# Optimization experiments

Measured on AMD Instinct MI355X. Metric: run time of the kernel, lower is better.

## Reference

```python
import jax, jax.numpy as jnp
import numpy as np

V, H, B, S, L = 32000, 512, 256, 128, 5
KAIMING_STD = float(np.sqrt(2.0 / H))  # kaiming_normal_ on (B,H): fan_in=H, gain=sqrt(2)
UNIF = float(1.0 / np.sqrt(H))         # torch LSTMCell/Linear default init scale


def setup_inputs() -> dict:
    key = jax.random.key(0)
    ks = jax.random.split(key, 12)
    x = jax.random.randint(ks[0], (B, S), 0, V)
    h0 = jax.random.normal(ks[1], (L, B, H), jnp.float32) * KAIMING_STD
    c0 = jax.random.normal(ks[2], (L, B, H), jnp.float32) * KAIMING_STD
    emb = jax.random.normal(ks[3], (V, H), jnp.float32)
    emb = emb.at[0].set(0.0)  # padding_idx=0
    W_ih = jax.random.uniform(ks[4], (L, 4 * H, H), jnp.float32, -UNIF, UNIF)
    W_hh = jax.random.uniform(ks[5], (L, 4 * H, H), jnp.float32, -UNIF, UNIF)
    b_ih = jax.random.uniform(ks[6], (L, 4 * H), jnp.float32, -UNIF, UNIF)
    b_hh = jax.random.uniform(ks[7], (L, 4 * H), jnp.float32, -UNIF, UNIF)
    W_out = jax.random.uniform(ks[8], (V, H), jnp.float32, -UNIF, UNIF)
    b_out = jax.random.uniform(ks[9], (V,), jnp.float32, -UNIF, UNIF)
    return {"x": x, "h0": h0, "c0": c0, "emb": emb, "W_ih": W_ih, "W_hh": W_hh,
            "b_ih": b_ih, "b_hh": b_hh, "W_out": W_out, "b_out": b_out}


def reference(x, h0, c0, emb, W_ih, W_hh, b_ih, b_hh, W_out, b_out):
    e = emb[x]                      # (B, S, H)
    seq = e.reshape(S, B, H)        # faithful replica of torch .view(S, B, -1) memory reinterpretation

    def step(carry, xt):
        h, c = carry                # each (L, B, H)
        inp = xt
        hs, cs = [], []
        for l in range(L):
            gates = inp @ W_ih[l].T + b_ih[l] + h[l] @ W_hh[l].T + b_hh[l]  # (B, 4H)
            i, f, g, o = jnp.split(gates, 4, axis=-1)
            i = jax.nn.sigmoid(i)
            f = jax.nn.sigmoid(f)
            g = jnp.tanh(g)
            o = jax.nn.sigmoid(o)
            cn = f * c[l] + i * g
            hn = o * jnp.tanh(cn)
            hs.append(hn)
            cs.append(cn)
            inp = hn
        return (jnp.stack(hs), jnp.stack(cs)), None

    (h, c), _ = jax.lax.scan(step, (h0, c0), seq)
    return h[L - 1] @ W_out.T + b_out  # (B, V)
```

## Files before the change

kernel.cpp:

```cpp
#include <hip/hip_runtime.h>
#include <hip/hip_bf16.h>

#define VOCAB 32000
#define HID 512
#define BATCH 256
#define SEQ 128
#define NL 5
#define BH (BATCH*HID)
#define G4H (4*HID)
#define NBLK 160

typedef __attribute__((ext_vector_type(8))) short short8;
typedef __attribute__((ext_vector_type(4))) float float4v;
typedef __attribute__((ext_vector_type(4))) unsigned int uint4v;

__device__ __forceinline__ float sigmoid_f(float x) {
    return 1.f / (1.f + __expf(-x));
}
__device__ __forceinline__ float tanh_f(float x) {
    float ax = fabsf(x);
    float e = __expf(2.f * ax);
    float t = 1.f - 2.f / (e + 1.f);
    return copysignf(t, x);
}
__device__ __forceinline__ short bf16bits(float f) {
    union { __hip_bfloat16 b; short s; } u;
    u.b = __float2bfloat16(f);
    return u.s;
}
__device__ __forceinline__ short8 load8f(const float* p) {
    float4v lo = *(const float4v*)p;
    float4v hi = *(const float4v*)(p + 4);
    short8 r;
    r[0] = bf16bits(lo[0]); r[1] = bf16bits(lo[1]);
    r[2] = bf16bits(lo[2]); r[3] = bf16bits(lo[3]);
    r[4] = bf16bits(hi[0]); r[5] = bf16bits(hi[1]);
    r[6] = bf16bits(hi[2]); r[7] = bf16bits(hi[3]);
    return r;
}
__device__ __forceinline__ short8 load8b(const __hip_bfloat16* p) {
    return *(const short8*)p;
}

#if __has_builtin(__builtin_amdgcn_make_buffer_rsrc) && \
    __has_builtin(__builtin_amdgcn_raw_buffer_load_b128) && \
    __has_builtin(__builtin_amdgcn_raw_buffer_store_b128)
#define USE_BUFFER_OPS 1
typedef __amdgpu_buffer_rsrc_t srd_t;
__device__ __forceinline__ srd_t make_srd(const void* p) {
    return __builtin_amdgcn_make_buffer_rsrc(const_cast<void*>(p), (short)0,
                                             0xFFFFFFFFu, 0x00020000);
}
__device__ __forceinline__ short8 bload16(srd_t srd, int voff, int soff) {
    union { uint4v u; short8 s; } c;
    c.u = __builtin_amdgcn_raw_buffer_load_b128(srd, voff, soff, 17);
    return c.s;
}
__device__ __forceinline__ void bstore16(short8 v, srd_t srd, int voff) {
    union { uint4v u; short8 s; } c; c.s = v;
    __builtin_amdgcn_raw_buffer_store_b128(c.u, srd, voff, 0, 17);
}
#else
#define USE_BUFFER_OPS 0
typedef const char* srd_t;
__device__ __forceinline__ srd_t make_srd(const void* p) {
    return (const char*)p;
}
__device__ __forceinline__ short8 bload16(srd_t srd, int voff, int soff) {
    const char* base = srd + voff + soff;
    union { unsigned long long q[2]; short8 s; } u;
    u.q[0] = __hip_atomic_load((const unsigned long long*)base,
                               __ATOMIC_RELAXED, __HIP_MEMORY_SCOPE_AGENT);
    u.q[1] = __hip_atomic_load((const unsigned long long*)(base + 8),
                               __ATOMIC_RELAXED, __HIP_MEMORY_SCOPE_AGENT);
    return u.s;
}
__device__ __forceinline__ void bstore16(short8 v, srd_t srd, int voff) {
    char* base = const_cast<char*>(srd) + voff;
    union { unsigned long long q[2]; short8 s; } u; u.s = v;
    __hip_atomic_store((unsigned long long*)base, u.q[0],
                       __ATOMIC_RELAXED, __HIP_MEMORY_SCOPE_AGENT);
    __hip_atomic_store((unsigned long long*)(base + 8), u.q[1],
                       __ATOMIC_RELAXED, __HIP_MEMORY_SCOPE_AGENT);
}
#endif

__device__ __forceinline__ size_t hidx(int p, int l, int j, int m, int c) {
    return ((((size_t)p * NL + l) * 32 + j) * 256 + m) * 16 + c;
}

__global__ void init_state_k(const float* __restrict__ h0,
                             __hip_bfloat16* __restrict__ hbuf,
                             int* __restrict__ done) {
    int i = blockIdx.x * 256 + threadIdx.x;
    int l = i / BH, r = i % BH;
    int m = r >> 9, col = r & 511;
    hbuf[hidx(1, l, col >> 4, m, col & 15)] = __float2bfloat16(h0[i]);
    if (blockIdx.x == 0 && threadIdx.x < NL) done[threadIdx.x * 64] = 0;
}

__global__ __launch_bounds__(1024) void lstm_persist_k(
    const int* __restrict__ x,
    const float* __restrict__ emb,
    const float* __restrict__ W_ih,
    const float* __restrict__ W_hh,
    const float* __restrict__ b_ih,
    const float* __restrict__ b_hh,
    const float* __restrict__ c0,
    __hip_bfloat16* __restrict__ hbuf,
    int* __restrict__ done)
{
    __shared__ short lw[65536];
    __shared__ short8 xch[16][32];

    const int tid = threadIdx.x;
    const int xcd = blockIdx.x & 7;
    const int ixc = blockIdx.x >> 3;
    const int slot = xcd * 20 + ixc;
    const int l = slot >> 5;
    const int j = slot & 31;
    const int jbase = j << 4;

    const int wave = tid >> 6, lane = tid & 63;
    const int quad = lane >> 4, l16 = lane & 15;
    const int m16 = wave << 4;

    const float* Wg[2] = { W_ih + (size_t)l * G4H * HID,
                           W_hh + (size_t)l * G4H * HID };

    for (int e = tid; e < 8192; e += 1024) {
        int row = e >> 6;
        int kc  = (e & 63) << 3;
        int gemm = row >> 6, r2 = row & 63, g = r2 >> 4, rl = r2 & 15;
        const float* src = Wg[gemm] + (size_t)(g * HID + jbase + rl) * HID + kc;
        short8 v = load8f(src);
        int kt = kc >> 5, q = (kc >> 3) & 3;
        int fragslot = ((gemm * 4 + g) * 16 + kt) * 64 + (q * 16 + rl);
        *(short8*)&lw[(size_t)fragslot * 8] = v;
    }

    const int jj = jbase + l16;
    float bias[4], c_r[4];
#pragma unroll
    for (int g = 0; g < 4; ++g)
        bias[g] = b_ih[l * G4H + g * HID + jj] + b_hh[l * G4H + g * HID + jj];
#pragma unroll
    for (int r = 0; r < 4; ++r)
        c_r[r] = c0[(size_t)l * BH + (size_t)(m16 + quad * 4 + r) * HID + jj];

    const short* lwb = lw + (size_t)lane * 8;
    const int shi = quad >> 1;
    const int abyte = (int)(((m16 + l16) * 16 + (quad & 1) * 8) * 2)
                    + shi * 8192;
    const srd_t hsrd = make_srd(hbuf);

    __syncthreads();

    for (int t = 0; t < SEQ; ++t) {
        if (tid == 0) {
            if (l > 0) {
                int need = 32 * (t + 1);
                while (__hip_atomic_load(&done[(l - 1) * 64], __ATOMIC_RELAXED,
                                         __HIP_MEMORY_SCOPE_AGENT) < need)
                    __builtin_amdgcn_s_sleep(1);
            }
            if (t > 0) {
                int need = 32 * t;
                while (__hip_atomic_load(&done[l * 64], __ATOMIC_RELAXED,
                                         __HIP_MEMORY_SCOPE_AGENT) < need)
                    __builtin_amdgcn_s_sleep(1);
            }
            if (l < NL - 1 && t >= 2) {
                int need = 32 * (t - 1);
                while (__hip_atomic_load(&done[(l + 1) * 64], __ATOMIC_RELAXED,
                                         __HIP_MEMORY_SCOPE_AGENT) < need)
                    __builtin_amdgcn_s_sleep(1);
            }
        }
        __syncthreads();

        const int p = t & 1, pm1 = p ^ 1;
        const int vpr = (int)(2 * hidx(pm1, l, 0, 0, 0)) + abyte;

        float4v acc[4];
#pragma unroll
        for (int g = 0; g < 4; ++g) acc[g] = (float4v){0.f, 0.f, 0.f, 0.f};

        if (l == 0) {
            int tok = x[t * BATCH + m16 + l16];
            const float* ar = emb + (size_t)tok * HID;
            short8 ah[4];
#pragma unroll
            for (int d = 0; d < 4; ++d)
                ah[d] = bload16(hsrd, vpr, d * 16384);
#pragma unroll
            for (int kt = 0; kt < 16; ++kt) {
                short8 a_in = load8f(ar + kt * 32 + quad * 8);
                short8 a_h = ah[kt & 3];
                if (kt + 4 < 16)
                    ah[kt & 3] = bload16(hsrd, vpr, (kt + 4) * 16384);
#pragma unroll
                for (int g = 0; g < 4; ++g) {
                    short8 b0 = *(const short8*)(lwb + (size_t)(g * 16 + kt) * 512);
                    short8 b1 = *(const short8*)(lwb + (size_t)((4 + g) * 16 + kt) * 512);
                    acc[g] = __builtin_amdgcn_mfma_f32_16x16x32_bf16(a_in, b0, acc[g], 0, 0, 0);
                    acc[g] = __builtin_amdgcn_mfma_f32_16x16x32_bf16(a_h,  b1, acc[g], 0, 0, 0);
                }
            }
        } else {
            const int vin = (int)(2 * hidx(p, l - 1, 0, 0, 0)) + abyte;
            short8 ai[4], ah[4];
#pragma unroll
            for (int d = 0; d < 4; ++d) {
                ai[d] = bload16(hsrd, vin, d * 16384);
                ah[d] = bload16(hsrd, vpr, d * 16384);
            }
#pragma unroll
            for (int kt = 0; kt < 16; ++kt) {
                short8 a_in = ai[kt & 3];
                short8 a_h  = ah[kt & 3];
                if (kt + 4 < 16) {
                    ai[kt & 3] = bload16(hsrd, vin, (kt + 4) * 16384);
                    ah[kt & 3] = bload16(hsrd, vpr, (kt + 4) * 16384);
                }
#pragma unroll
                for (int g = 0; g < 4; ++g) {
                    short8 b0 = *(const short8*)(lwb + (size_t)(g * 16 + kt) * 512);
                    short8 b1 = *(const short8*)(lwb + (size_t)((4 + g) * 16 + kt) * 512);
                    acc[g] = __builtin_amdgcn_mfma_f32_16x16x32_bf16(a_in, b0, acc[g], 0, 0, 0);
                    acc[g] = __builtin_amdgcn_mfma_f32_16x16x32_bf16(a_h,  b1, acc[g], 0, 0, 0);
                }
            }
        }

        short* xp = (short*)&xch[wave];
#pragma unroll
        for (int r = 0; r < 4; ++r) {
            float iv = sigmoid_f(acc[0][r] + bias[0]);
            float fv = sigmoid_f(acc[1][r] + bias[1]);
            float gv = tanh_f(acc[2][r] + bias[2]);
            float ov = sigmoid_f(acc[3][r] + bias[3]);
            c_r[r] = fv * c_r[r] + iv * gv;
            xp[(quad * 4 + r) * 16 + l16] = bf16bits(ov * tanh_f(c_r[r]));
        }
        __builtin_amdgcn_wave_barrier();
        if (lane < 32) {
            short8 v = *(const short8*)&xp[lane * 8];
            int vout = (int)(2 * hidx(p, l, j, m16, 0)) + lane * 16;
            bstore16(v, hsrd, vout);
        }

        __syncthreads();
        if (tid == 0)
            __hip_atomic_fetch_add(&done[l * 64], 1, __ATOMIC_RELEASE,
                                   __HIP_MEMORY_SCOPE_AGENT);
    }
}

__global__ __launch_bounds__(512) void out_gemm_k(
    const __hip_bfloat16* __restrict__ hbuf,
    const float* __restrict__ W_out,
    const float* __restrict__ b_out,
    float* __restrict__ out)
{
    const int nb = blockIdx.x;
    const int tid = threadIdx.x;
    const int wave = tid >> 6, lane = tid & 63;
    const int quad = lane >> 4, l16 = lane & 15;
    const int nt = wave & 3, mh = wave >> 2;

    const __hip_bfloat16* hfin = hbuf + hidx(1, NL - 1, 0, 0, 0);
    const int shi = quad >> 1;
    const size_t coff = (size_t)(quad & 1) * 8;

    const int ncol = nb * 64 + nt * 16 + l16;
    const float* brow = W_out + (size_t)ncol * HID;

    float4v acc[8];
#pragma unroll
    for (int mt = 0; mt < 8; ++mt) acc[mt] = (float4v){0.f, 0.f, 0.f, 0.f};

#pragma unroll 2
    for (int kt = 0; kt < 16; ++kt) {
        short8 b = load8f(brow + kt * 32 + quad * 8);
        const __hip_bfloat16* abase =
            hfin + (size_t)(2 * kt + shi) * 4096 + coff;
#pragma unroll
        for (int mt = 0; mt < 8; ++mt) {
            short8 a = load8b(abase + (size_t)(mh * 128 + mt * 16 + l16) * 16);
            acc[mt] = __builtin_amdgcn_mfma_f32_16x16x32_bf16(a, b, acc[mt], 0, 0, 0);
        }
    }

    float bo = b_out[ncol];
#pragma unroll
    for (int mt = 0; mt < 8; ++mt) {
#pragma unroll
        for (int r = 0; r < 4; ++r) {
            int m = mh * 128 + mt * 16 + quad * 4 + r;
            out[(size_t)m * VOCAB + ncol] = acc[mt][r] + bo;
        }
    }
}

extern "C" void kernel_launch(void* const* d_in, const int* in_sizes, int n_in,
                              void* d_out, int out_size, void* d_ws, size_t ws_size,
                              hipStream_t stream) {
    const int* x        = (const int*)d_in[0];
    const float* h0     = (const float*)d_in[1];
    const float* c0     = (const float*)d_in[2];
    const float* emb    = (const float*)d_in[3];
    const float* W_ih   = (const float*)d_in[4];
    const float* W_hh   = (const float*)d_in[5];
    const float* b_ih   = (const float*)d_in[6];
    const float* b_hh   = (const float*)d_in[7];
    const float* W_out  = (const float*)d_in[8];
    const float* b_out  = (const float*)d_in[9];
    float* out          = (float*)d_out;

    __hip_bfloat16* hbuf = (__hip_bfloat16*)d_ws;
    int* done = (int*)((char*)d_ws + (size_t)2 * NL * BH * sizeof(__hip_bfloat16));

    init_state_k<<<(NL * BH) / 256, 256, 0, stream>>>(h0, hbuf, done);

    lstm_persist_k<<<NBLK, 1024, 0, stream>>>(x, emb, W_ih, W_hh, b_ih, b_hh,
                                              c0, hbuf, done);

    out_gemm_k<<<VOCAB / 64, 512, 0, stream>>>(hbuf, W_out, b_out, out);
}
```

Before: 3.196 ms.

## Store per-timestep hidden states to drop downstream-layer backpressure wait

Measured after the change: 3.014 ms. 5.7% less time.

```diff
diff --git a/kernel.cpp b/kernel.cpp
--- a/kernel.cpp
+++ b/kernel.cpp
@@ -45,7 +45,6 @@
 #if __has_builtin(__builtin_amdgcn_make_buffer_rsrc) && \
     __has_builtin(__builtin_amdgcn_raw_buffer_load_b128) && \
     __has_builtin(__builtin_amdgcn_raw_buffer_store_b128)
-#define USE_BUFFER_OPS 1
 typedef __amdgpu_buffer_rsrc_t srd_t;
 __device__ __forceinline__ srd_t make_srd(const void* p) {
     return __builtin_amdgcn_make_buffer_rsrc(const_cast<void*>(p), (short)0,
@@ -61,7 +60,6 @@
     __builtin_amdgcn_raw_buffer_store_b128(c.u, srd, voff, 0, 17);
 }
 #else
-#define USE_BUFFER_OPS 0
 typedef const char* srd_t;
 __device__ __forceinline__ srd_t make_srd(const void* p) {
     return (const char*)p;
@@ -85,20 +83,31 @@
 }
 #endif
 
-__device__ __forceinline__ size_t hidx(int p, int l, int j, int m, int c) {
-    return ((((size_t)p * NL + l) * 32 + j) * 256 + m) * 16 + c;
+__host__ __device__ constexpr size_t hidx(int s, int l, int j, int m, int c) {
+    return ((((size_t)s * NL + l) * 32 + j) * 256 + m) * 16 + c;
+}
+
+template<int BIGWS>
+__device__ __forceinline__ short8 hload(const __hip_bfloat16* hbuf, srd_t srd,
+                                        size_t off, int d) {
+    if constexpr (BIGWS) {
+        return *(const short8*)((const char*)hbuf + off + (size_t)d * 16384);
+    } else {
+        return bload16(srd, (int)off, d * 16384);
+    }
 }
 
 __global__ void init_state_k(const float* __restrict__ h0,
                              __hip_bfloat16* __restrict__ hbuf,
-                             int* __restrict__ done) {
+                             int* __restrict__ done, int islot) {
     int i = blockIdx.x * 256 + threadIdx.x;
     int l = i / BH, r = i % BH;
     int m = r >> 9, col = r & 511;
-    hbuf[hidx(1, l, col >> 4, m, col & 15)] = __float2bfloat16(h0[i]);
+    hbuf[hidx(islot, l, col >> 4, m, col & 15)] = __float2bfloat16(h0[i]);
     if (blockIdx.x == 0 && threadIdx.x < NL) done[threadIdx.x * 64] = 0;
 }
 
+template<int BIGWS>
 __global__ __launch_bounds__(1024) void lstm_persist_k(
     const int* __restrict__ x,
     const float* __restrict__ emb,
@@ -150,8 +159,8 @@
 
     const short* lwb = lw + (size_t)lane * 8;
     const int shi = quad >> 1;
-    const int abyte = (int)(((m16 + l16) * 16 + (quad & 1) * 8) * 2)
-                    + shi * 8192;
+    const size_t abyte = (size_t)(((m16 + l16) * 16 + (quad & 1) * 8) * 2)
+                       + (size_t)shi * 8192;
     const srd_t hsrd = make_srd(hbuf);
 
     __syncthreads();
@@ -170,17 +179,23 @@
                                          __HIP_MEMORY_SCOPE_AGENT) < need)
                     __builtin_amdgcn_s_sleep(1);
             }
-            if (l < NL - 1 && t >= 2) {
-                int need = 32 * (t - 1);
-                while (__hip_atomic_load(&done[(l + 1) * 64], __ATOMIC_RELAXED,
-                                         __HIP_MEMORY_SCOPE_AGENT) < need)
-                    __builtin_amdgcn_s_sleep(1);
+            if constexpr (!BIGWS) {
+                if (l < NL - 1 && t >= 2) {
+                    int need = 32 * (t - 1);
+                    while (__hip_atomic_load(&done[(l + 1) * 64], __ATOMIC_RELAXED,
+                                             __HIP_MEMORY_SCOPE_AGENT) < need)
+                        __builtin_amdgcn_s_sleep(1);
+                }
             }
         }
         __syncthreads();
 
         const int p = t & 1, pm1 = p ^ 1;
-        const int vpr = (int)(2 * hidx(pm1, l, 0, 0, 0)) + abyte;
+        const int rslot_prev = BIGWS ? t : pm1;
+        const int rslot_in   = BIGWS ? (t + 1) : p;
+        const int wslot      = BIGWS ? (t + 1) : p;
+
+        const size_t vpr = 2 * hidx(rslot_prev, l, 0, 0, 0) + abyte;
 
         float4v acc[4];
 #pragma unroll
@@ -192,13 +207,13 @@
             short8 ah[4];
 #pragma unroll
             for (int d = 0; d < 4; ++d)
-                ah[d] = bload16(hsrd, vpr, d * 16384);
+                ah[d] = hload<BIGWS>(hbuf, hsrd, vpr, d);
 #pragma unroll
             for (int kt = 0; kt < 16; ++kt) {
                 short8 a_in = load8f(ar + kt * 32 + quad * 8);
                 short8 a_h = ah[kt & 3];
                 if (kt + 4 < 16)
-                    ah[kt & 3] = bload16(hsrd, vpr, (kt + 4) * 16384);
+                    ah[kt & 3] = hload<BIGWS>(hbuf, hsrd, vpr, kt + 4);
 #pragma unroll
                 for (int g = 0; g < 4; ++g) {
                     short8 b0 = *(const short8*)(lwb + (size_t)(g * 16 + kt) * 512);
@@ -208,20 +223,20 @@
                 }
             }
         } else {
-            const int vin = (int)(2 * hidx(p, l - 1, 0, 0, 0)) + abyte;
+            const size_t vin = 2 * hidx(rslot_in, l - 1, 0, 0, 0) + abyte;
             short8 ai[4], ah[4];
 #pragma unroll
             for (int d = 0; d < 4; ++d) {
-                ai[d] = bload16(hsrd, vin, d * 16384);
-                ah[d] = bload16(hsrd, vpr, d * 16384);
+                ai[d] = hload<BIGWS>(hbuf, hsrd, vin, d);
+                ah[d] = hload<BIGWS>(hbuf, hsrd, vpr, d);
             }
 #pragma unroll
             for (int kt = 0; kt < 16; ++kt) {
                 short8 a_in = ai[kt & 3];
                 short8 a_h  = ah[kt & 3];
                 if (kt + 4 < 16) {
-                    ai[kt & 3] = bload16(hsrd, vin, (kt + 4) * 16384);
-                    ah[kt & 3] = bload16(hsrd, vpr, (kt + 4) * 16384);
+                    ai[kt & 3] = hload<BIGWS>(hbuf, hsrd, vin, kt + 4);
+                    ah[kt & 3] = hload<BIGWS>(hbuf, hsrd, vpr, kt + 4);
                 }
 #pragma unroll
                 for (int g = 0; g < 4; ++g) {
@@ -246,7 +261,7 @@
         __builtin_amdgcn_wave_barrier();
         if (lane < 32) {
             short8 v = *(const short8*)&xp[lane * 8];
-            int vout = (int)(2 * hidx(p, l, j, m16, 0)) + lane * 16;
+            int vout = (int)(2 * hidx(wslot, l, j, m16, 0)) + lane * 16;
             bstore16(v, hsrd, vout);
         }
 
@@ -258,7 +273,7 @@
 }
 
 __global__ __launch_bounds__(512) void out_gemm_k(
-    const __hip_bfloat16* __restrict__ hbuf,
+    const __hip_bfloat16* __restrict__ hfin,
     const float* __restrict__ W_out,
     const float* __restrict__ b_out,
     float* __restrict__ out)
@@ -269,7 +284,6 @@
     const int quad = lane >> 4, l16 = lane & 15;
     const int nt = wave & 3, mh = wave >> 2;
 
-    const __hip_bfloat16* hfin = hbuf + hidx(1, NL - 1, 0, 0, 0);
     const int shi = quad >> 1;
     const size_t coff = (size_t)(quad & 1) * 8;
 
@@ -319,12 +333,23 @@
     float* out          = (float*)d_out;
 
     __hip_bfloat16* hbuf = (__hip_bfloat16*)d_ws;
-    int* done = (int*)((char*)d_ws + (size_t)2 * NL * BH * sizeof(__hip_bfloat16));
-
-    init_state_k<<<(NL * BH) / 256, 256, 0, stream>>>(h0, hbuf, done);
-
-    lstm_persist_k<<<NBLK, 1024, 0, stream>>>(x, emb, W_ih, W_hh, b_ih, b_hh,
-                                              c0, hbuf, done);
-
-    out_gemm_k<<<VOCAB / 64, 512, 0, stream>>>(hbuf, W_out, b_out, out);
-}
+
+    const size_t hbytes_big = (size_t)(SEQ + 1) * NL * BH * sizeof(__hip_bfloat16);
+    const bool big = ws_size >= hbytes_big + 4096;
+
+    if (big) {
+        int* done = (int*)((char*)d_ws + hbytes_big);
+        init_state_k<<<(NL * BH) / 256, 256, 0, stream>>>(h0, hbuf, done, 0);
+        lstm_persist_k<1><<<NBLK, 1024, 0, stream>>>(x, emb, W_ih, W_hh, b_ih,
+                                                     b_hh, c0, hbuf, done);
+        out_gemm_k<<<VOCAB / 64, 512, 0, stream>>>(
+            hbuf + hidx(SEQ, NL - 1, 0, 0, 0), W_out, b_out, out);
+    } else {
+        int* done = (int*)((char*)d_ws + (size_t)2 * NL * BH * sizeof(__hip_bfloat16));
+        init_state_k<<<(NL * BH) / 256, 256, 0, stream>>>(h0, hbuf, done, 1);
+        lstm_persist_k<0><<<NBLK, 1024, 0, stream>>>(x, emb, W_ih, W_hh, b_ih,
+                                                     b_hh, c0, hbuf, done);
+        out_gemm_k<<<VOCAB / 64, 512, 0, stream>>>(
+            hbuf + hidx(1, NL - 1, 0, 0, 0), W_out, b_out, out);
+    }
+}
```

## Assign LSTM layers to XCDs dynamically and keep recurrent state in XCD-local L2

Applied to the files above, without the earlier changes.

Measured after the change: 3.569 ms. 11.6% more time.

```diff
diff --git a/kernel.cpp b/kernel.cpp
--- a/kernel.cpp
+++ b/kernel.cpp
@@ -8,7 +8,15 @@
 #define NL 5
 #define BH (BATCH*HID)
 #define G4H (4*HID)
-#define NBLK 160
+#define NBLK_LAUNCH 256
+
+#define LAYB  (32*256*16*2)
+#define SLOTB (NL*LAYB)
+
+#define F_DONE(l)   ((l)*64)
+#define F_CLAIM(x)  (384 + (x)*8)
+#define F_CHECKIN   512
+#define F_SPILL     576
 
 typedef __attribute__((ext_vector_type(8))) short short8;
 typedef __attribute__((ext_vector_type(4))) float float4v;
@@ -45,7 +53,6 @@
 #if __has_builtin(__builtin_amdgcn_make_buffer_rsrc) && \
     __has_builtin(__builtin_amdgcn_raw_buffer_load_b128) && \
     __has_builtin(__builtin_amdgcn_raw_buffer_store_b128)
-#define USE_BUFFER_OPS 1
 typedef __amdgpu_buffer_rsrc_t srd_t;
 __device__ __forceinline__ srd_t make_srd(const void* p) {
     return __builtin_amdgcn_make_buffer_rsrc(const_cast<void*>(p), (short)0,
@@ -56,12 +63,16 @@
     c.u = __builtin_amdgcn_raw_buffer_load_b128(srd, voff, soff, 17);
     return c.s;
 }
+__device__ __forceinline__ short8 bload16_l2(srd_t srd, int voff, int soff) {
+    union { uint4v u; short8 s; } c;
+    c.u = __builtin_amdgcn_raw_buffer_load_b128(srd, voff, soff, 1);
+    return c.s;
+}
 __device__ __forceinline__ void bstore16(short8 v, srd_t srd, int voff) {
     union { uint4v u; short8 s; } c; c.s = v;
     __builtin_amdgcn_raw_buffer_store_b128(c.u, srd, voff, 0, 17);
 }
 #else
-#define USE_BUFFER_OPS 0
 typedef const char* srd_t;
 __device__ __forceinline__ srd_t make_srd(const void* p) {
     return (const char*)p;
@@ -75,6 +86,9 @@
                                __ATOMIC_RELAXED, __HIP_MEMORY_SCOPE_AGENT);
     return u.s;
 }
+__device__ __forceinline__ short8 bload16_l2(srd_t srd, int voff, int soff) {
+    return bload16(srd, voff, soff);
+}
 __device__ __forceinline__ void bstore16(short8 v, srd_t srd, int voff) {
     char* base = const_cast<char*>(srd) + voff;
     union { unsigned long long q[2]; short8 s; } u; u.s = v;
@@ -85,18 +99,181 @@
 }
 #endif
 
-__device__ __forceinline__ size_t hidx(int p, int l, int j, int m, int c) {
-    return ((((size_t)p * NL + l) * 32 + j) * 256 + m) * 16 + c;
+__host__ __device__ constexpr size_t hidx(int s, int l, int j, int m, int c) {
+    return ((((size_t)s * NL + l) * 32 + j) * 256 + m) * 16 + c;
 }
 
 __global__ void init_state_k(const float* __restrict__ h0,
                              __hip_bfloat16* __restrict__ hbuf,
-                             int* __restrict__ done) {
+                             __hip_bfloat16* __restrict__ hloc,
+                             int* __restrict__ flags) {
     int i = blockIdx.x * 256 + threadIdx.x;
     int l = i / BH, r = i % BH;
     int m = r >> 9, col = r & 511;
-    hbuf[hidx(1, l, col >> 4, m, col & 15)] = __float2bfloat16(h0[i]);
-    if (blockIdx.x == 0 && threadIdx.x < NL) done[threadIdx.x * 64] = 0;
+    size_t o = hidx(1, l, col >> 4, m, col & 15);
+    __hip_bfloat16 v = __float2bfloat16(h0[i]);
+    hbuf[o] = v;
+    hloc[o] = v;
+    if (blockIdx.x == 0) {
+        flags[threadIdx.x] = 0;
+        flags[threadIdx.x + 256] = 0;
+        flags[threadIdx.x + 512] = 0;
+    }
+}
+
+template<int FAST>
+__device__ __forceinline__ void lstm_run(
+    const int* __restrict__ x, const float* __restrict__ emb,
+    const float* __restrict__ W_ih, const float* __restrict__ W_hh,
+    const float* __restrict__ b_ih, const float* __restrict__ b_hh,
+    const float* __restrict__ c0,
+    __hip_bfloat16* __restrict__ hbuf,
+    __hip_bfloat16* __restrict__ hloc,
+    int* __restrict__ flags, int l, int j,
+    short* __restrict__ lw, short8 (*__restrict__ xch)[32])
+{
+    const int tid = threadIdx.x;
+    const int jbase = j << 4;
+    const int wave = tid >> 6, lane = tid & 63;
+    const int quad = lane >> 4, l16 = lane & 15;
+    const int m16 = wave << 4;
+
+    const float* Wg[2] = { W_ih + (size_t)l * G4H * HID,
+                           W_hh + (size_t)l * G4H * HID };
+
+    for (int e = tid; e < 8192; e += 1024) {
+        int row = e >> 6;
+        int kc  = (e & 63) << 3;
+        int gemm = row >> 6, r2 = row & 63, g = r2 >> 4, rl = r2 & 15;
+        const float* src = Wg[gemm] + (size_t)(g * HID + jbase + rl) * HID + kc;
+        short8 v = load8f(src);
+        int kt = kc >> 5, q = (kc >> 3) & 3;
+        int fragslot = ((gemm * 4 + g) * 16 + kt) * 64 + (q * 16 + rl);
+        *(short8*)&lw[(size_t)fragslot * 8] = v;
+    }
+
+    const int jj = jbase + l16;
+    float bias[4], c_r[4];
+#pragma unroll
+    for (int g = 0; g < 4; ++g)
+        bias[g] = b_ih[l * G4H + g * HID + jj] + b_hh[l * G4H + g * HID + jj];
+#pragma unroll
+    for (int r = 0; r < 4; ++r)
+        c_r[r] = c0[(size_t)l * BH + (size_t)(m16 + quad * 4 + r) * HID + jj];
+
+    const short* lwb = lw + (size_t)lane * 8;
+    const int shi = quad >> 1;
+    const int abyte = ((m16 + l16) * 16 + (quad & 1) * 8) * 2 + shi * 8192;
+    const srd_t hsrd = make_srd(hbuf);
+    const srd_t lsrd = make_srd(hloc);
+
+    __syncthreads();
+
+    for (int t = 0; t < SEQ; ++t) {
+        if (tid == 0) {
+            if (l > 0) {
+                int need = 32 * (t + 1);
+                while (__hip_atomic_load(&flags[F_DONE(l - 1)], __ATOMIC_RELAXED,
+                                         __HIP_MEMORY_SCOPE_AGENT) < need)
+                    __builtin_amdgcn_s_sleep(1);
+            }
+            if (t > 0) {
+                int need = 32 * t;
+                while (__hip_atomic_load(&flags[F_DONE(l)], __ATOMIC_RELAXED,
+                                         __HIP_MEMORY_SCOPE_AGENT) < need)
+                    __builtin_amdgcn_s_sleep(1);
+            }
+            if (l < NL - 1 && t >= 2) {
+                int need = 32 * (t - 1);
+                while (__hip_atomic_load(&flags[F_DONE(l + 1)], __ATOMIC_RELAXED,
+                                         __HIP_MEMORY_SCOPE_AGENT) < need)
+                    __builtin_amdgcn_s_sleep(1);
+            }
+        }
+        __syncthreads();
+
+        const int p = t & 1, pm1 = p ^ 1;
+        const int vpr = pm1 * SLOTB + l * LAYB + abyte;
+
+        float4v acc[4];
+#pragma unroll
+        for (int g = 0; g < 4; ++g) acc[g] = (float4v){0.f, 0.f, 0.f, 0.f};
+
+        if (l == 0) {
+            int tok = x[t * BATCH + m16 + l16];
+            const float* ar = emb + (size_t)tok * HID;
+            short8 ah[4];
+#pragma unroll
+            for (int d = 0; d < 4; ++d)
+                ah[d] = FAST ? bload16_l2(lsrd, vpr, d * 16384)
+                             : bload16(hsrd, vpr, d * 16384);
+#pragma unroll
+            for (int kt = 0; kt < 16; ++kt) {
+                short8 a_in = load8f(ar + kt * 32 + quad * 8);
+                short8 a_h = ah[kt & 3];
+                if (kt + 4 < 16)
+                    ah[kt & 3] = FAST ? bload16_l2(lsrd, vpr, (kt + 4) * 16384)
+                                      : bload16(hsrd, vpr, (kt + 4) * 16384);
+#pragma unroll
+                for (int g = 0; g < 4; ++g) {
+                    short8 b0 = *(const short8*)(lwb + (size_t)(g * 16 + kt) * 512);
+                    short8 b1 = *(const short8*)(lwb + (size_t)((4 + g) * 16 + kt) * 512);
+                    acc[g] = __builtin_amdgcn_mfma_f32_16x16x32_bf16(a_in, b0, acc[g], 0, 0, 0);
+                    acc[g] = __builtin_amdgcn_mfma_f32_16x16x32_bf16(a_h,  b1, acc[g], 0, 0, 0);
+                }
+            }
+        } else {
+            const int vin = p * SLOTB + (l - 1) * LAYB + abyte;
+            short8 ai[4], ah[4];
+#pragma unroll
+            for (int d = 0; d < 4; ++d) {
+                ai[d] = bload16(hsrd, vin, d * 16384);
+                ah[d] = FAST ? bload16_l2(lsrd, vpr, d * 16384)
+                             : bload16(hsrd, vpr, d * 16384);
+            }
+#pragma unroll
+            for (int kt = 0; kt < 16; ++kt) {
+                short8 a_in = ai[kt & 3];
+                short8 a_h  = ah[kt & 3];
+                if (kt + 4 < 16) {
+                    ai[kt & 3] = bload16(hsrd, vin, (kt + 4) * 16384);
+                    ah[kt & 3] = FAST ? bload16_l2(lsrd, vpr, (kt + 4) * 16384)
+                                      : bload16(hsrd, vpr, (kt + 4) * 16384);
+                }
+#pragma unroll
+                for (int g = 0; g < 4; ++g) {
+                    short8 b0 = *(const short8*)(lwb + (size_t)(g * 16 + kt) * 512);
+                    short8 b1 = *(const short8*)(lwb + (size_t)((4 + g) * 16 + kt) * 512);
+                    acc[g] = __builtin_amdgcn_mfma_f32_16x16x32_bf16(a_in, b0, acc[g], 0, 0, 0);
+                    acc[g] = __builtin_amdgcn_mfma_f32_16x16x32_bf16(a_h,  b1, acc[g], 0, 0, 0);
+                }
+            }
+        }
+
+        short* xp = (short*)&xch[wave];
+#pragma unroll
+        for (int r = 0; r < 4; ++r) {
+            float iv = sigmoid_f(acc[0][r] + bias[0]);
+            float fv = sigmoid_f(acc[1][r] + bias[1]);
+            float gv = tanh_f(acc[2][r] + bias[2]);
+            float ov = sigmoid_f(acc[3][r] + bias[3]);
+            c_r[r] = fv * c_r[r] + iv * gv;
+            xp[(quad * 4 + r) * 16 + l16] = bf16bits(ov * tanh_f(c_r[r]));
+        }
+        __builtin_amdgcn_wave_barrier();
+        if (lane < 32) {
+            short8 v = *(const short8*)&xp[lane * 8];
+            int vout = p * SLOTB + l * LAYB + j * 8192 + m16 * 32 + lane * 16;
+            bstore16(v, hsrd, vout);
+            if (FAST)
+                *(short8*)((char*)hloc + vout) = v;
+        }
+
+        __syncthreads();
+        if (tid == 0)
+            __hip_atomic_fetch_add(&flags[F_DONE(l)], 1, __ATOMIC_RELEASE,
+                                   __HIP_MEMORY_SCOPE_AGENT);
+    }
 }
 
 __global__ __launch_bounds__(1024) void lstm_persist_k(
@@ -108,157 +285,66 @@
     const float* __restrict__ b_hh,
     const float* __restrict__ c0,
     __hip_bfloat16* __restrict__ hbuf,
-    int* __restrict__ done)
+    __hip_bfloat16* __restrict__ hloc,
+    int* __restrict__ flags)
 {
     __shared__ short lw[65536];
     __shared__ short8 xch[16][32];
+    __shared__ int info[3];
 
     const int tid = threadIdx.x;
-    const int xcd = blockIdx.x & 7;
-    const int ixc = blockIdx.x >> 3;
-    const int slot = xcd * 20 + ixc;
-    const int l = slot >> 5;
-    const int j = slot & 31;
-    const int jbase = j << 4;
-
-    const int wave = tid >> 6, lane = tid & 63;
-    const int quad = lane >> 4, l16 = lane & 15;
-    const int m16 = wave << 4;
-
-    const float* Wg[2] = { W_ih + (size_t)l * G4H * HID,
-                           W_hh + (size_t)l * G4H * HID };
-
-    for (int e = tid; e < 8192; e += 1024) {
-        int row = e >> 6;
-        int kc  = (e & 63) << 3;
-        int gemm = row >> 6, r2 = row & 63, g = r2 >> 4, rl = r2 & 15;
-        const float* src = Wg[gemm] + (size_t)(g * HID + jbase + rl) * HID + kc;
-        short8 v = load8f(src);
-        int kt = kc >> 5, q = (kc >> 3) & 3;
-        int fragslot = ((gemm * 4 + g) * 16 + kt) * 64 + (q * 16 + rl);
-        *(short8*)&lw[(size_t)fragslot * 8] = v;
-    }
-
-    const int jj = jbase + l16;
-    float bias[4], c_r[4];
-#pragma unroll
-    for (int g = 0; g < 4; ++g)
-        bias[g] = b_ih[l * G4H + g * HID + jj] + b_hh[l * G4H + g * HID + jj];
-#pragma unroll
-    for (int r = 0; r < 4; ++r)
-        c_r[r] = c0[(size_t)l * BH + (size_t)(m16 + quad * 4 + r) * HID + jj];
-
-    const short* lwb = lw + (size_t)lane * 8;
-    const int shi = quad >> 1;
-    const int abyte = (int)(((m16 + l16) * 16 + (quad & 1) * 8) * 2)
-                    + shi * 8192;
-    const srd_t hsrd = make_srd(hbuf);
-
+    if (tid == 0) {
+        unsigned xcc;
+#if __has_builtin(__builtin_amdgcn_s_getreg)
+        xcc = (unsigned)__builtin_amdgcn_s_getreg(63508) & 7u;
+#else
+        xcc = (unsigned)(blockIdx.x & 7);
+#endif
+        int pos = __hip_atomic_fetch_add(&flags[F_CLAIM(xcc)], 1,
+                                         __ATOMIC_RELAXED, __HIP_MEMORY_SCOPE_AGENT);
+        __hip_atomic_fetch_add(&flags[F_CHECKIN], 1,
+                               __ATOMIC_RELEASE, __HIP_MEMORY_SCOPE_AGENT);
+        while (__hip_atomic_load(&flags[F_CHECKIN], __ATOMIC_RELAXED,
+                                 __HIP_MEMORY_SCOPE_AGENT) < NBLK_LAUNCH)
+            __builtin_amdgcn_s_sleep(8);
+        __builtin_amdgcn_fence(__ATOMIC_ACQUIRE, "agent");
+
+        int cl[5]; int fast = 1;
+        for (int i = 0; i < 5; ++i) {
+            int c = __hip_atomic_load(&flags[F_CLAIM(i)], __ATOMIC_RELAXED,
+                                      __HIP_MEMORY_SCOPE_AGENT);
+            cl[i] = c > 32 ? 32 : c;
+            if (cl[i] < 32) fast = 0;
+        }
+        int layer = -1, jslice = 0;
+        if (xcc < 5 && pos < 32) {
+            layer = (int)xcc; jslice = pos;
+        } else {
+            int k = __hip_atomic_fetch_add(&flags[F_SPILL], 1,
+                                           __ATOMIC_RELAXED, __HIP_MEMORY_SCOPE_AGENT);
+            int cum = 0;
+            for (int i = 0; i < 5; ++i) {
+                int d = 32 - cl[i];
+                if (k < cum + d) { layer = i; jslice = cl[i] + (k - cum); break; }
+                cum += d;
+            }
+        }
+        info[0] = layer; info[1] = jslice; info[2] = fast;
+    }
     __syncthreads();
-
-    for (int t = 0; t < SEQ; ++t) {
-        if (tid == 0) {
-            if (l > 0) {
-                int need = 32 * (t + 1);
-                while (__hip_atomic_load(&done[(l - 1) * 64], __ATOMIC_RELAXED,
-                                         __HIP_MEMORY_SCOPE_AGENT) < need)
-                    __builtin_amdgcn_s_sleep(1);
-            }
-            if (t > 0) {
-                int need = 32 * t;
-                while (__hip_atomic_load(&done[l * 64], __ATOMIC_RELAXED,
-                                         __HIP_MEMORY_SCOPE_AGENT) < need)
-                    __builtin_amdgcn_s_sleep(1);
-            }
-            if (l < NL - 1 && t >= 2) {
-                int need = 32 * (t - 1);
-                while (__hip_atomic_load(&done[(l + 1) * 64], __ATOMIC_RELAXED,
-                                         __HIP_MEMORY_SCOPE_AGENT) < need)
-                    __builtin_amdgcn_s_sleep(1);
-            }
-        }
-        __syncthreads();
-
-        const int p = t & 1, pm1 = p ^ 1;
-        const int vpr = (int)(2 * hidx(pm1, l, 0, 0, 0)) + abyte;
-
-        float4v acc[4];
-#pragma unroll
-        for (int g = 0; g < 4; ++g) acc[g] = (float4v){0.f, 0.f, 0.f, 0.f};
-
-        if (l == 0) {
-            int tok = x[t * BATCH + m16 + l16];
-            const float* ar = emb + (size_t)tok * HID;
-            short8 ah[4];
-#pragma unroll
-            for (int d = 0; d < 4; ++d)
-                ah[d] = bload16(hsrd, vpr, d * 16384);
-#pragma unroll
-            for (int kt = 0; kt < 16; ++kt) {
-                short8 a_in = load8f(ar + kt * 32 + quad * 8);
-                short8 a_h = ah[kt & 3];
-                if (kt + 4 < 16)
-                    ah[kt & 3] = bload16(hsrd, vpr, (kt + 4) * 16384);
-#pragma unroll
-                for (int g = 0; g < 4; ++g) {
-                    short8 b0 = *(const short8*)(lwb + (size_t)(g * 16 + kt) * 512);
-                    short8 b1 = *(const short8*)(lwb + (size_t)((4 + g) * 16 + kt) * 512);
-                    acc[g] = __builtin_amdgcn_mfma_f32_16x16x32_bf16(a_in, b0, acc[g], 0, 0, 0);
-                    acc[g] = __builtin_amdgcn_mfma_f32_16x16x32_bf16(a_h,  b1, acc[g], 0, 0, 0);
-                }
-            }
-        } else {
-            const int vin = (int)(2 * hidx(p, l - 1, 0, 0, 0)) + abyte;
-            short8 ai[4], ah[4];
-#pragma unroll
-            for (int d = 0; d < 4; ++d) {
-                ai[d] = bload16(hsrd, vin, d * 16384);
-                ah[d] = bload16(hsrd, vpr, d * 16384);
-            }
-#pragma unroll
-            for (int kt = 0; kt < 16; ++kt) {
-                short8 a_in = ai[kt & 3];
-                short8 a_h  = ah[kt & 3];
-                if (kt + 4 < 16) {
-                    ai[kt & 3] = bload16(hsrd, vin, (kt + 4) * 16384);
-                    ah[kt & 3] = bload16(hsrd, vpr, (kt + 4) * 16384);
-                }
-#pragma unroll
-                for (int g = 0; g < 4; ++g) {
-                    short8 b0 = *(const short8*)(lwb + (size_t)(g * 16 + kt) * 512);
-                    short8 b1 = *(const short8*)(lwb + (size_t)((4 + g) * 16 + kt) * 512);
-                    acc[g] = __builtin_amdgcn_mfma_f32_16x16x32_bf16(a_in, b0, acc[g], 0, 0, 0);
-                    acc[g] = __builtin_amdgcn_mfma_f32_16x16x32_bf16(a_h,  b1, acc[g], 0, 0, 0);
-                }
-            }
-        }
-
-        short* xp = (short*)&xch[wave];
-#pragma unroll
-        for (int r = 0; r < 4; ++r) {
-            float iv = sigmoid_f(acc[0][r] + bias[0]);
-            float fv = sigmoid_f(acc[1][r] + bias[1]);
-            float gv = tanh_f(acc[2][r] + bias[2]);
-            float ov = sigmoid_f(acc[3][r] + bias[3]);
-            c_r[r] = fv * c_r[r] + iv * gv;
-            xp[(quad * 4 + r) * 16 + l16] = bf16bits(ov * tanh_f(c_r[r]));
-        }
-        __builtin_amdgcn_wave_barrier();
-        if (lane < 32) {
-            short8 v = *(const short8*)&xp[lane * 8];
-            int vout = (int)(2 * hidx(p, l, j, m16, 0)) + lane * 16;
-            bstore16(v, hsrd, vout);
-        }
-
-        __syncthreads();
-        if (tid == 0)
-            __hip_atomic_fetch_add(&done[l * 64], 1, __ATOMIC_RELEASE,
-                                   __HIP_MEMORY_SCOPE_AGENT);
-    }
+    const int l = info[0], j = info[1], fast = info[2];
+    if (l < 0) return;
+
+    if (fast)
+        lstm_run<1>(x, emb, W_ih, W_hh, b_ih, b_hh, c0, hbuf, hloc, flags,
+                    l, j, lw, xch);
+    else
+        lstm_run<0>(x, emb, W_ih, W_hh, b_ih, b_hh, c0, hbuf, hloc, flags,
+                    l, j, lw, xch);
 }
 
 __global__ __launch_bounds__(512) void out_gemm_k(
-    const __hip_bfloat16* __restrict__ hbuf,
+    const __hip_bfloat16* __restrict__ hfin,
     const float* __restrict__ W_out,
     const float* __restrict__ b_out,
     float* __restrict__ out)
@@ -269,7 +355,6 @@
     const int quad = lane >> 4, l16 = lane & 15;
     const int nt = wave & 3, mh = wave >> 2;
 
-    const __hip_bfloat16* hfin = hbuf + hidx(1, NL - 1, 0, 0, 0);
     const int shi = quad >> 1;
     const size_t coff = (size_t)(quad & 1) * 8;
 
@@ -319,12 +404,14 @@
     float* out          = (float*)d_out;
 
     __hip_bfloat16* hbuf = (__hip_bfloat16*)d_ws;
-    int* done = (int*)((char*)d_ws + (size_t)2 * NL * BH * sizeof(__hip_bfloat16));
-
-    init_state_k<<<(NL * BH) / 256, 256, 0, stream>>>(h0, hbuf, done);
-
-    lstm_persist_k<<<NBLK, 1024, 0, stream>>>(x, emb, W_ih, W_hh, b_ih, b_hh,
-                                              c0, hbuf, done);
-
-    out_gemm_k<<<VOCAB / 64, 512, 0, stream>>>(hbuf, W_out, b_out, out);
-}
+    int* flags = (int*)((char*)d_ws + (size_t)2 * SLOTB);
+    __hip_bfloat16* hloc = (__hip_bfloat16*)d_out;
+
+    init_state_k<<<(NL * BH) / 256, 256, 0, stream>>>(h0, hbuf, hloc, flags);
+
+    lstm_persist_k<<<NBLK_LAUNCH, 1024, 0, stream>>>(x, emb, W_ih, W_hh, b_ih,
+                                                     b_hh, c0, hbuf, hloc, flags);
+
+    out_gemm_k<<<VOCAB / 64, 512, 0, stream>>>(
+        hbuf + hidx(1, NL - 1, 0, 0, 0), W_out, b_out, out);
+}
```

## Replace per-layer counters with per-wave flags and a 4-slot hidden-state ring

Applied to the files above, without the earlier changes.

Result: slower. 8.727 ms (+173.0%).

```diff
diff --git a/kernel.cpp b/kernel.cpp
--- a/kernel.cpp
+++ b/kernel.cpp
@@ -9,6 +9,10 @@
 #define BH (BATCH*HID)
 #define G4H (4*HID)
 #define NBLK 160
+
+#define LAYB  (32*256*16*2)
+#define SLOTB (NL*LAYB)
+#define NSLOT 4
 
 typedef __attribute__((ext_vector_type(8))) short short8;
 typedef __attribute__((ext_vector_type(4))) float float4v;
@@ -45,7 +49,6 @@
 #if __has_builtin(__builtin_amdgcn_make_buffer_rsrc) && \
     __has_builtin(__builtin_amdgcn_raw_buffer_load_b128) && \
     __has_builtin(__builtin_amdgcn_raw_buffer_store_b128)
-#define USE_BUFFER_OPS 1
 typedef __amdgpu_buffer_rsrc_t srd_t;
 __device__ __forceinline__ srd_t make_srd(const void* p) {
     return __builtin_amdgcn_make_buffer_rsrc(const_cast<void*>(p), (short)0,
@@ -61,7 +64,6 @@
     __builtin_amdgcn_raw_buffer_store_b128(c.u, srd, voff, 0, 17);
 }
 #else
-#define USE_BUFFER_OPS 0
 typedef const char* srd_t;
 __device__ __forceinline__ srd_t make_srd(const void* p) {
     return (const char*)p;
@@ -85,18 +87,18 @@
 }
 #endif
 
-__device__ __forceinline__ size_t hidx(int p, int l, int j, int m, int c) {
-    return ((((size_t)p * NL + l) * 32 + j) * 256 + m) * 16 + c;
+__host__ __device__ constexpr size_t hidx(int s, int l, int j, int m, int c) {
+    return ((((size_t)s * NL + l) * 32 + j) * 256 + m) * 16 + c;
 }
 
 __global__ void init_state_k(const float* __restrict__ h0,
-                             __hip_bfloat16* __restrict__ hbuf,
-                             int* __restrict__ done) {
+                             __hip_bfloat16* __restrict__ hring,
+                             int* __restrict__ flags) {
     int i = blockIdx.x * 256 + threadIdx.x;
     int l = i / BH, r = i % BH;
     int m = r >> 9, col = r & 511;
-    hbuf[hidx(1, l, col >> 4, m, col & 15)] = __float2bfloat16(h0[i]);
-    if (blockIdx.x == 0 && threadIdx.x < NL) done[threadIdx.x * 64] = 0;
+    hring[hidx(0, l, col >> 4, m, col & 15)] = __float2bfloat16(h0[i]);
+    if (blockIdx.x < 16) flags[blockIdx.x * 256 + threadIdx.x] = 0;
 }
 
 __global__ __launch_bounds__(1024) void lstm_persist_k(
@@ -107,8 +109,9 @@
     const float* __restrict__ b_ih,
     const float* __restrict__ b_hh,
     const float* __restrict__ c0,
-    __hip_bfloat16* __restrict__ hbuf,
-    int* __restrict__ done)
+    __hip_bfloat16* __restrict__ hring,
+    __hip_bfloat16* __restrict__ hfin,
+    int* __restrict__ flags)
 {
     __shared__ short lw[65536];
     __shared__ short8 xch[16][32];
@@ -150,37 +153,38 @@
 
     const short* lwb = lw + (size_t)lane * 8;
     const int shi = quad >> 1;
-    const int abyte = (int)(((m16 + l16) * 16 + (quad & 1) * 8) * 2)
-                    + shi * 8192;
-    const srd_t hsrd = make_srd(hbuf);
+    const int abyte = ((m16 + l16) * 16 + (quad & 1) * 8) * 2 + shi * 8192;
+    const srd_t rsrd = make_srd(hring);
+    const srd_t fsrd = make_srd(hfin);
+
+    const int* fprev = flags + (((l - 1) * 16 + wave) << 5);
+    const int* fown  = flags + ((l * 16 + wave) << 5);
+    const int* fnext = flags + (((l + 1) * 16 + wave) << 5);
+    int* fmy = flags + ((l * 16 + wave) << 5) + j;
+    const int lane31 = lane & 31;
 
     __syncthreads();
 
     for (int t = 0; t < SEQ; ++t) {
-        if (tid == 0) {
-            if (l > 0) {
-                int need = 32 * (t + 1);
-                while (__hip_atomic_load(&done[(l - 1) * 64], __ATOMIC_RELAXED,
-                                         __HIP_MEMORY_SCOPE_AGENT) < need)
-                    __builtin_amdgcn_s_sleep(1);
-            }
-            if (t > 0) {
-                int need = 32 * t;
-                while (__hip_atomic_load(&done[l * 64], __ATOMIC_RELAXED,
-                                         __HIP_MEMORY_SCOPE_AGENT) < need)
-                    __builtin_amdgcn_s_sleep(1);
-            }
-            if (l < NL - 1 && t >= 2) {
-                int need = 32 * (t - 1);
-                while (__hip_atomic_load(&done[(l + 1) * 64], __ATOMIC_RELAXED,
-                                         __HIP_MEMORY_SCOPE_AGENT) < need)
-                    __builtin_amdgcn_s_sleep(1);
-            }
-        }
-        __syncthreads();
-
-        const int p = t & 1, pm1 = p ^ 1;
-        const int vpr = (int)(2 * hidx(pm1, l, 0, 0, 0)) + abyte;
+        for (;;) {
+            bool ok = true;
+            if (l > 0)
+                ok &= __hip_atomic_load(&fprev[lane31], __ATOMIC_RELAXED,
+                                        __HIP_MEMORY_SCOPE_AGENT) >= t + 1;
+            if (t > 0)
+                ok &= __hip_atomic_load(&fown[lane31], __ATOMIC_RELAXED,
+                                        __HIP_MEMORY_SCOPE_AGENT) >= t;
+            if (l < NL - 1 && t >= 3)
+                ok &= __hip_atomic_load(&fnext[lane31], __ATOMIC_RELAXED,
+                                        __HIP_MEMORY_SCOPE_AGENT) >= t - 2;
+            if (__all(ok)) break;
+            __builtin_amdgcn_s_sleep(2);
+        }
+
+        const int rs_prev = t & (NSLOT - 1);
+        const int rs_in   = (t + 1) & (NSLOT - 1);
+        const int ws_     = (t + 1) & (NSLOT - 1);
+        const int vpr = rs_prev * SLOTB + l * LAYB + abyte;
 
         float4v acc[4];
 #pragma unroll
@@ -192,13 +196,13 @@
             short8 ah[4];
 #pragma unroll
             for (int d = 0; d < 4; ++d)
-                ah[d] = bload16(hsrd, vpr, d * 16384);
+                ah[d] = bload16(rsrd, vpr, d * 16384);
 #pragma unroll
             for (int kt = 0; kt < 16; ++kt) {
                 short8 a_in = load8f(ar + kt * 32 + quad * 8);
                 short8 a_h = ah[kt & 3];
                 if (kt + 4 < 16)
-                    ah[kt & 3] = bload16(hsrd, vpr, (kt + 4) * 16384);
+                    ah[kt & 3] = bload16(rsrd, vpr, (kt + 4) * 16384);
 #pragma unroll
                 for (int g = 0; g < 4; ++g) {
                     short8 b0 = *(const short8*)(lwb + (size_t)(g * 16 + kt) * 512);
@@ -208,20 +212,20 @@
                 }
             }
         } else {
-            const int vin = (int)(2 * hidx(p, l - 1, 0, 0, 0)) + abyte;
+            const int vin = rs_in * SLOTB + (l - 1) * LAYB + abyte;
             short8 ai[4], ah[4];
 #pragma unroll
             for (int d = 0; d < 4; ++d) {
-                ai[d] = bload16(hsrd, vin, d * 16384);
-                ah[d] = bload16(hsrd, vpr, d * 16384);
+                ai[d] = bload16(rsrd, vin, d * 16384);
+                ah[d] = bload16(rsrd, vpr, d * 16384);
             }
 #pragma unroll
             for (int kt = 0; kt < 16; ++kt) {
                 short8 a_in = ai[kt & 3];
                 short8 a_h  = ah[kt & 3];
                 if (kt + 4 < 16) {
-                    ai[kt & 3] = bload16(hsrd, vin, (kt + 4) * 16384);
-                    ah[kt & 3] = bload16(hsrd, vpr, (kt + 4) * 16384);
+                    ai[kt & 3] = bload16(rsrd, vin, (kt + 4) * 16384);
+                    ah[kt & 3] = bload16(rsrd, vpr, (kt + 4) * 16384);
                 }
 #pragma unroll
                 for (int g = 0; g < 4; ++g) {
@@ -246,19 +250,19 @@
         __builtin_amdgcn_wave_barrier();
         if (lane < 32) {
             short8 v = *(const short8*)&xp[lane * 8];
-            int vout = (int)(2 * hidx(p, l, j, m16, 0)) + lane * 16;
-            bstore16(v, hsrd, vout);
-        }
-
-        __syncthreads();
-        if (tid == 0)
-            __hip_atomic_fetch_add(&done[l * 64], 1, __ATOMIC_RELEASE,
-                                   __HIP_MEMORY_SCOPE_AGENT);
+            int voutc = j * 8192 + m16 * 32 + lane * 16;
+            bstore16(v, rsrd, ws_ * SLOTB + l * LAYB + voutc);
+            if (l == NL - 1 && t == SEQ - 1)
+                bstore16(v, fsrd, voutc);
+        }
+        if (lane == 0)
+            __hip_atomic_store(fmy, t + 1, __ATOMIC_RELEASE,
+                               __HIP_MEMORY_SCOPE_AGENT);
     }
 }
 
 __global__ __launch_bounds__(512) void out_gemm_k(
-    const __hip_bfloat16* __restrict__ hbuf,
+    const __hip_bfloat16* __restrict__ hfin,
     const float* __restrict__ W_out,
     const float* __restrict__ b_out,
     float* __restrict__ out)
@@ -269,7 +273,6 @@
     const int quad = lane >> 4, l16 = lane & 15;
     const int nt = wave & 3, mh = wave >> 2;
 
-    const __hip_bfloat16* hfin = hbuf + hidx(1, NL - 1, 0, 0, 0);
     const int shi = quad >> 1;
     const size_t coff = (size_t)(quad & 1) * 8;
 
@@ -318,13 +321,14 @@
     const float* b_out  = (const float*)d_in[9];
     float* out          = (float*)d_out;
 
-    __hip_bfloat16* hbuf = (__hip_bfloat16*)d_ws;
-    int* done = (int*)((char*)d_ws + (size_t)2 * NL * BH * sizeof(__hip_bfloat16));
-
-    init_state_k<<<(NL * BH) / 256, 256, 0, stream>>>(h0, hbuf, done);
+    __hip_bfloat16* hring = (__hip_bfloat16*)d_out;
+    int* flags = (int*)((char*)d_out + (size_t)NSLOT * SLOTB);
+    __hip_bfloat16* hfin = (__hip_bfloat16*)d_ws;
+
+    init_state_k<<<(NL * BH) / 256, 256, 0, stream>>>(h0, hring, flags);
 
     lstm_persist_k<<<NBLK, 1024, 0, stream>>>(x, emb, W_ih, W_hh, b_ih, b_hh,
-                                              c0, hbuf, done);
-
-    out_gemm_k<<<VOCAB / 64, 512, 0, stream>>>(hbuf, W_out, b_out, out);
-}
+                                              c0, hring, hfin, flags);
+
+    out_gemm_k<<<VOCAB / 64, 512, 0, stream>>>(hfin, W_out, b_out, out);
+}
```
